# Kernel tuning notes

Measured on AMD Instinct MI355X. Metric: run time of the kernel, lower is better.

The kernel has to match this reference:

```python
import jax, jax.numpy as jnp
import numpy as np

N_EMBD = 1024
N_HEAD = 16
STRIDE = 128
C = 8
SEQ = 2048
BATCH = 2


def _sparse_causal_mask(nd, ns, stride, c, dtype):
    # Faithful vectorization of _sparse_attention_mask:
    # column j is globally visible if (j % stride) >= stride - c (the last c
    # columns of each stride block), each query also sees its own stride block,
    # and everything is causally masked (j <= q).
    j = jnp.arange(ns)
    q = jnp.arange(ns)[:, None]
    col_sel = (j % stride) >= (stride - c)          # strided summary columns
    same_block = (j[None, :] // stride) == (q // stride)  # local block
    causal = j[None, :] <= q
    mask = ((col_sel[None, :] | same_block) & causal).astype(dtype)
    return mask[ns - nd:]


def setup_inputs() -> dict:
    key = jax.random.key(0)
    k1, k2, k3 = jax.random.split(key, 3)
    inputs = jax.random.normal(k1, (BATCH, SEQ, N_EMBD), dtype=jnp.float32)
    w_attn = jax.random.normal(k2, (N_EMBD, 3 * N_EMBD), dtype=jnp.float32) * 0.02
    b_attn = jnp.zeros((3 * N_EMBD,), dtype=jnp.float32)
    proj_std = 0.02 / np.sqrt(2 * 24)  # n_layer = 24
    w_proj = jax.random.normal(k3, (N_EMBD, N_EMBD), dtype=jnp.float32) * proj_std
    b_proj = jnp.zeros((N_EMBD,), dtype=jnp.float32)
    return {"inputs": inputs, "w_attn": w_attn, "b_attn": b_attn,
            "w_proj": w_proj, "b_proj": b_proj}


def reference(inputs, w_attn, b_attn, w_proj, b_proj):
    B, S, E = inputs.shape
    H = N_HEAD
    D = E // H
    qkv = inputs @ w_attn + b_attn                     # [B,S,3E]
    q, k, v = jnp.split(qkv, 3, axis=-1)
    def split_heads(x):
        return x.reshape(B, S, H, D).transpose(0, 2, 1, 3)  # [B,H,S,D]
    q, k, v = split_heads(q), split_heads(k), split_heads(v)
    present = jnp.stack([k, v], axis=1)                # [B,2,H,S,D]
    scale = jnp.asarray(D, q.dtype) ** 0.5
    w = jnp.einsum('bhqd,bhkd->bhqk', q, k) / scale    # [B,H,S,S]
    mask = _sparse_causal_mask(S, S, STRIDE, C, w.dtype)
    w = w * mask - 1e10 * (1.0 - mask)
    p = jax.nn.softmax(w, axis=-1).astype(v.dtype)
    h = jnp.einsum('bhqk,bhkd->bhqd', p, v)            # [B,H,S,D]
    h = h.transpose(0, 2, 1, 3).reshape(B, S, E)       # merge heads
    h = h @ w_proj + b_proj
    # dropout p=0.0 (eval) -> identity
    return (h, present)
```

## Files before the change

kernel.cpp:

```cpp
#include <hip/hip_runtime.h>
#include <stdint.h>

typedef unsigned short u16;
typedef unsigned int u32;
typedef __attribute__((ext_vector_type(4))) float f32x4;
typedef __attribute__((ext_vector_type(4))) u16 u16x4;
typedef __attribute__((ext_vector_type(8))) __bf16 bf16x8;

__device__ __forceinline__ u16 f2bf(float f) {
  u32 u = __builtin_bit_cast(u32, f);
  u = (u + 0x7FFFu + ((u >> 16) & 1u)) >> 16;
  return (u16)u;
}

__device__ __forceinline__ void gload_lds16(const void* g, void* l) {
  __builtin_amdgcn_global_load_lds(
      (const __attribute__((address_space(1))) void*)(uintptr_t)(g),
      (__attribute__((address_space(3))) void*)(u32)(uintptr_t)(l),
      16, 0, 0);
}

__global__ __launch_bounds__(256) void k_prep(
    const float* __restrict__ x, u16* __restrict__ xbf,
    const float* __restrict__ wa, u16* __restrict__ wat,
    const float* __restrict__ wp, u16* __restrict__ wpt) {
  __shared__ float tile[32][33];
  const int bid = blockIdx.x, t = threadIdx.x;
  if (bid < 4096) {
    int i = bid * 256 + t;
    f32x4 v = ((const f32x4*)x)[i];
    u16x4 o = { f2bf(v.x), f2bf(v.y), f2bf(v.z), f2bf(v.w) };
    ((u16x4*)xbf)[i] = o;
    return;
  }
  const float* in;
  u16* out;
  int n0, k0, N;
  if (bid < 4096 + 3072) {
    int idx = bid - 4096;
    in = wa; out = wat; N = 3072;
    n0 = (idx % 96) * 32; k0 = (idx / 96) * 32;
  } else {
    int idx = bid - 7168;
    in = wp; out = wpt; N = 1024;
    n0 = (idx & 31) * 32; k0 = (idx >> 5) * 32;
  }
  int c = t & 31, r0 = t >> 5;
#pragma unroll
  for (int i = 0; i < 4; ++i)
    tile[r0 + i * 8][c] = in[(size_t)(k0 + r0 + i * 8) * N + n0 + c];
  __syncthreads();
  int on = t >> 3, ok = (t & 7) * 4;
  u16x4 o = { f2bf(tile[ok + 0][on]), f2bf(tile[ok + 1][on]),
              f2bf(tile[ok + 2][on]), f2bf(tile[ok + 3][on]) };
  *(u16x4*)&out[(size_t)(n0 + on) * 1024 + k0 + ok] = o;
}

__global__ __launch_bounds__(256) void k_kv(const float* __restrict__ present,
                                            u16* __restrict__ kbf,
                                            u16* __restrict__ vtw) {
  __shared__ float tile[32][33];
  const int bid = blockIdx.x, t = threadIdx.x;
  if (bid >= 4096) {
    int i = bid - 4096;
    size_t idx = (size_t)i * 256 + t;
    size_t b = idx >> 19, off = idx & ((1u << 19) - 1);
    f32x4 v = ((const f32x4*)present)[b * (1u << 20) + off];
    u16x4 o = { f2bf(v.x), f2bf(v.y), f2bf(v.z), f2bf(v.w) };
    ((u16x4*)kbf)[idx] = o;
    return;
  }
  int bh = bid >> 7, rem = bid & 127;
  int s0 = (rem >> 1) * 32, d0 = (rem & 1) * 32;
  int b = bh >> 4, h = bh & 15;
  const float* vsrc = present + (((size_t)(b * 2 + 1) * 16 + h) * 2048) * 64;
  u16* vdst = vtw + ((size_t)bh * 64) * 2048;
  int c = t & 31, r0 = t >> 5;
#pragma unroll
  for (int i = 0; i < 4; ++i)
    tile[r0 + i * 8][c] = vsrc[(size_t)(s0 + r0 + i * 8) * 64 + d0 + c];
  __syncthreads();
  int on = t >> 3, ok = (t & 7) * 4;
  u16x4 o = { f2bf(tile[ok + 0][on]), f2bf(tile[ok + 1][on]),
              f2bf(tile[ok + 2][on]), f2bf(tile[ok + 3][on]) };
  *(u16x4*)&vdst[(size_t)(d0 + on) * 2048 + s0 + ok] = o;
}

__global__ __launch_bounds__(512, 1) void k_gemm256(
    const u16* __restrict__ A, const u16* __restrict__ Bt,
    const float* __restrict__ bias, u16* __restrict__ outq,
    float* __restrict__ outp) {
  __shared__ u16 a_lds[2][256 * 64];
  __shared__ u16 b_lds[2][256 * 64];
  const int t = threadIdx.x;
  const int lane = t & 63, w = t >> 6;
  const int cc = lane & 15, g = lane >> 4;
  const int wr = w >> 2, wc = w & 3;

  int flat = blockIdx.y * 12 + blockIdx.x;
  flat = (flat & 7) * 24 + (flat >> 3);
  const int m0 = (flat / 12) * 256, n0 = (flat % 12) * 256;

  const int srow = t >> 3;
  const int scolb = (t & 7) * 16;
  const size_t pitch = 2048;

  auto stage = [&](int bi, int kt) {
#pragma unroll
    for (int hh = 0; hh < 2; ++hh)
#pragma unroll
      for (int i = 0; i < 2; ++i) {
        int row = hh * 128 + i * 64 + srow;
        int sw = scolb ^ ((row & 7) << 4);
        gload_lds16((const char*)A + (size_t)(m0 + row) * pitch + kt * 128 + sw,
                    (char*)a_lds[bi] + row * 128 + scolb);
        gload_lds16((const char*)Bt + (size_t)(n0 + row) * pitch + kt * 128 + sw,
                    (char*)b_lds[bi] + row * 128 + scolb);
      }
  };

  f32x4 acc[8][4] = {};

  stage(0, 0);
  stage(1, 1);
  __syncthreads();

  for (int kt = 0; kt < 16; ++kt) {
    const int bi = kt & 1;
    if (kt >= 1 && kt < 15) stage(1 - bi, kt + 1);

    bf16x8 bfr[4][2];
#pragma unroll
    for (int nf = 0; nf < 4; ++nf) {
      int row = wc * 64 + nf * 16 + cc;
#pragma unroll
      for (int kk = 0; kk < 2; ++kk)
        bfr[nf][kk] = *(const bf16x8*)((const char*)b_lds[bi] + row * 128 +
                                       ((kk * 64 + g * 16) ^ ((row & 7) << 4)));
    }
#pragma unroll
    for (int q = 0; q < 4; ++q) {
      bf16x8 af[2][2];
#pragma unroll
      for (int mf = 0; mf < 2; ++mf) {
        int row = wr * 128 + q * 32 + mf * 16 + cc;
#pragma unroll
        for (int kk = 0; kk < 2; ++kk)
          af[mf][kk] = *(const bf16x8*)((const char*)a_lds[bi] + row * 128 +
                                        ((kk * 64 + g * 16) ^ ((row & 7) << 4)));
      }
      __builtin_amdgcn_s_setprio(1);
#pragma unroll
      for (int mf = 0; mf < 2; ++mf)
#pragma unroll
        for (int nf = 0; nf < 4; ++nf)
#pragma unroll
          for (int kk = 0; kk < 2; ++kk)
            acc[q * 2 + mf][nf] = __builtin_amdgcn_mfma_f32_16x16x32_bf16(
                af[mf][kk], bfr[nf][kk], acc[q * 2 + mf][nf], 0, 0, 0);
      __builtin_amdgcn_s_setprio(0);
    }
    if (kt < 15) __syncthreads();
  }

  float bv[4];
#pragma unroll
  for (int nf = 0; nf < 4; ++nf) bv[nf] = bias[n0 + wc * 64 + nf * 16 + cc];

#pragma unroll
  for (int q8 = 0; q8 < 8; ++q8)
#pragma unroll
    for (int nf = 0; nf < 4; ++nf) {
      int n = n0 + wc * 64 + nf * 16 + cc;
      int mb = m0 + wr * 128 + q8 * 16 + g * 4;
      float v[4];
#pragma unroll
      for (int j = 0; j < 4; ++j) v[j] = acc[q8][nf][j] + bv[nf];
      if (n < 1024) {
#pragma unroll
        for (int j = 0; j < 4; ++j) outq[(size_t)(mb + j) * 1024 + n] = f2bf(v[j]);
      } else {
        int n2 = n - 1024;
        int kv = n2 >> 10; n2 &= 1023;
        int hh = n2 >> 6, d = n2 & 63;
        int bb = mb >> 11, ss = mb & 2047;
        float* pr = outp + ((((size_t)bb * 2 + kv) * 16 + hh) * 2048 + ss) * 64 + d;
#pragma unroll
        for (int j = 0; j < 4; ++j) pr[(size_t)j * 64] = v[j];
      }
    }
}

template <int EPI, int BN>
__global__ __launch_bounds__(256) void k_gemm(
    const u16* __restrict__ A, const u16* __restrict__ Bt,
    const float* __restrict__ bias, u16* __restrict__ outq,
    float* __restrict__ outp, int M, int N, int K) {
  __shared__ u16 a_lds[128 * 64];
  __shared__ u16 b_lds[BN * 64];
  const int t = threadIdx.x;
  const int lane = t & 63, w = t >> 6;
  const int m0 = blockIdx.y * 128, n0 = blockIdx.x * BN;
  const int srow = t >> 3;
  const int scb = (t & 7) * 16;
  const int ssw = scb ^ ((srow & 7) << 4);
  const size_t pitch = (size_t)K * 2;
  const char* aS = (const char*)A + (size_t)(m0 + srow) * pitch + ssw;
  const char* bS = (const char*)Bt + (size_t)(n0 + srow) * pitch + ssw;
  char* al = (char*)a_lds + t * 16;
  char* bl = (char*)b_lds + t * 16;
  const int wm = (w >> 1) * 64, wn = (w & 1) * (BN / 2);
  const int cc = lane & 15, g = lane >> 4;
  constexpr int NF = BN / 32;

  f32x4 acc[4][NF] = {};

  for (int kt = 0; kt < K; kt += 64) {
    __syncthreads();
#pragma unroll
    for (int i = 0; i < 4; ++i)
      gload_lds16(aS + (size_t)kt * 2 + (size_t)i * 32 * pitch, al + i * 4096);
#pragma unroll
    for (int i = 0; i < BN / 32; ++i)
      gload_lds16(bS + (size_t)kt * 2 + (size_t)i * 32 * pitch, bl + i * 4096);
    __syncthreads();
#pragma unroll
    for (int kk = 0; kk < 2; ++kk) {
      bf16x8 af[4], bf_[NF];
#pragma unroll
      for (int mf = 0; mf < 4; ++mf) {
        int row = wm + mf * 16 + cc;
        af[mf] = *(const bf16x8*)((const char*)a_lds + row * 128 +
                                  ((kk * 64 + g * 16) ^ ((row & 7) << 4)));
      }
#pragma unroll
      for (int nf = 0; nf < NF; ++nf) {
        int row = wn + nf * 16 + cc;
        bf_[nf] = *(const bf16x8*)((const char*)b_lds + row * 128 +
                                   ((kk * 64 + g * 16) ^ ((row & 7) << 4)));
      }
#pragma unroll
      for (int mf = 0; mf < 4; ++mf)
#pragma unroll
        for (int nf = 0; nf < NF; ++nf)
          acc[mf][nf] = __builtin_amdgcn_mfma_f32_16x16x32_bf16(
              af[mf], bf_[nf], acc[mf][nf], 0, 0, 0);
    }
  }

  float bv[NF];
#pragma unroll
  for (int nf = 0; nf < NF; ++nf) bv[nf] = bias[n0 + wn + nf * 16 + cc];

#pragma unroll
  for (int mf = 0; mf < 4; ++mf)
#pragma unroll
    for (int nf = 0; nf < NF; ++nf) {
      int n = n0 + wn + nf * 16 + cc;
      int mb = m0 + wm + mf * 16 + g * 4;
      float v[4];
#pragma unroll
      for (int j = 0; j < 4; ++j) v[j] = acc[mf][nf][j] + bv[nf];
      if (EPI == 1) {
#pragma unroll
        for (int j = 0; j < 4; ++j) outp[(size_t)(mb + j) * N + n] = v[j];
      } else if (n < 1024) {
#pragma unroll
        for (int j = 0; j < 4; ++j) outq[(size_t)(mb + j) * 1024 + n] = f2bf(v[j]);
      } else {
        int n2 = n - 1024;
        int kv = n2 >> 10; n2 &= 1023;
        int hh = n2 >> 6, d = n2 & 63;
        int bb = mb >> 11, ss = mb & 2047;
        float* pr = outp + ((((size_t)bb * 2 + kv) * 16 + hh) * 2048 + ss) * 64 + d;
#pragma unroll
        for (int j = 0; j < 4; ++j) pr[(size_t)j * 64] = v[j];
      }
    }
}

__global__ __launch_bounds__(256) void k_attn(
    const u16* __restrict__ qws, const u16* __restrict__ kbf,
    const u16* __restrict__ vtw, u16* __restrict__ hws) {
  const int qb = blockIdx.x, h = blockIdx.y, b = blockIdx.z;
  const int t = threadIdx.x, lane = t & 63, w = t >> 6;
  const int cc = lane & 15, g = lane >> 4;

  __shared__ u16 k_lds[256 * 64];
  __shared__ u16 p_lds[4][32 * 72];
  __shared__ float rsum[4][32];

  const char* kh = (const char*)kbf + (size_t)(b * 16 + h) * (2048 * 128);
  const char* vh = (const char*)vtw + (size_t)(b * 16 + h) * (64 * 4096);

  {
    int rr = t >> 3, seg = (t & 7) * 16;
#pragma unroll
    for (int i = 0; i < 8; ++i) {
      int r = i * 32 + rr;
      int i2 = r - 128;
      int gr = (r < 128) ? (qb * 128 + r) : ((i2 >> 3) * 128 + 120 + (i2 & 7));
      gload_lds16(kh + (size_t)gr * 128 + (seg ^ ((r & 7) << 4)),
                  (char*)k_lds + i * 4096 + t * 16);
    }
  }

  bf16x8 qf_[2][2];
  {
    const char* qsrc = (const char*)qws +
        (size_t)(b * 2048 + qb * 128 + w * 32 + cc) * 2048 + h * 128 + g * 16;
#pragma unroll
    for (int qf = 0; qf < 2; ++qf)
#pragma unroll
      for (int kk = 0; kk < 2; ++kk)
        qf_[qf][kk] = *(const bf16x8*)(qsrc + (size_t)qf * 16 * 2048 + kk * 64);
  }
  __syncthreads();

  const int nsum = 8 * qb;
  f32x4 o_[2][4] = {};
  float lsum[2] = { 0.f, 0.f };

#pragma unroll 2
  for (int ch = 0; ch < 4; ++ch) {
    f32x4 s[4][2] = {};
#pragma unroll
    for (int kf2 = 0; kf2 < 4; ++kf2) {
      int row = ch * 64 + kf2 * 16 + cc;
      const char* kr = (const char*)k_lds + row * 128;
#pragma unroll
      for (int kk = 0; kk < 2; ++kk) {
        bf16x8 kfr = *(const bf16x8*)(kr + ((kk * 64 + g * 16) ^ ((cc & 7) << 4)));
#pragma unroll
        for (int qf = 0; qf < 2; ++qf)
          s[kf2][qf] = __builtin_amdgcn_mfma_f32_16x16x32_bf16(
              kfr, qf_[qf][kk], s[kf2][qf], 0, 0, 0);
      }
    }
#pragma unroll
    for (int qf = 0; qf < 2; ++qf) {
      int q_local = w * 32 + qf * 16 + cc;
#pragma unroll
      for (int kf2 = 0; kf2 < 4; ++kf2) {
#pragma unroll
        for (int j = 0; j < 4; ++j) {
          int key = ch * 64 + kf2 * 16 + g * 4 + j;
          bool vis = (key < 128) ? (key <= q_local) : (key - 128 < nsum);
          float p = vis ? exp2f(s[kf2][qf][j] * 0.180336884f) : 0.f;
          s[kf2][qf][j] = p;
          lsum[qf] += p;
        }
        u16x4 pw = { f2bf(s[kf2][qf][0]), f2bf(s[kf2][qf][1]),
                     f2bf(s[kf2][qf][2]), f2bf(s[kf2][qf][3]) };
        *(u16x4*)&p_lds[w][(qf * 16 + cc) * 72 + kf2 * 16 + g * 4] = pw;
      }
    }
#pragma unroll
    for (int kk = 0; kk < 2; ++kk) {
      bf16x8 pa[2], vb[4];
#pragma unroll
      for (int mf = 0; mf < 2; ++mf)
        pa[mf] = *(const bf16x8*)((const char*)p_lds[w] +
                                  (mf * 16 + cc) * 144 + kk * 64 + g * 16);
      int cb = (ch < 2) ? (qb * 256 + ch * 128 + kk * 64 + g * 16)
                        : (((ch - 2) * 8 + kk * 4 + g) * 256 + 240);
#pragma unroll
      for (int nf = 0; nf < 4; ++nf)
        vb[nf] = *(const bf16x8*)(vh + (size_t)(nf * 16 + cc) * 4096 + cb);
#pragma unroll
      for (int mf = 0; mf < 2; ++mf)
#pragma unroll
        for (int nf = 0; nf < 4; ++nf)
          o_[mf][nf] = __builtin_amdgcn_mfma_f32_16x16x32_bf16(pa[mf], vb[nf],
                                                               o_[mf][nf], 0, 0, 0);
    }
  }

#pragma unroll
  for (int qf = 0; qf < 2; ++qf) {
    float sum = lsum[qf];
    sum += __shfl_xor(sum, 16);
    sum += __shfl_xor(sum, 32);
    if (g == 0) rsum[w][qf * 16 + cc] = sum;
  }
#pragma unroll
  for (int mf = 0; mf < 2; ++mf)
#pragma unroll
    for (int j = 0; j < 4; ++j) {
      float inv = 1.0f / rsum[w][mf * 16 + g * 4 + j];
      size_t row = (size_t)(b * 2048 + qb * 128 + w * 32 + mf * 16 + g * 4 + j);
#pragma unroll
      for (int nf = 0; nf < 4; ++nf)
        hws[row * 1024 + h * 64 + nf * 16 + cc] = f2bf(o_[mf][nf][j] * inv);
    }
}

extern "C" void kernel_launch(void* const* d_in, const int* in_sizes, int n_in,
                              void* d_out, int out_size, void* d_ws, size_t ws_size,
                              hipStream_t stream) {
  const float* x      = (const float*)d_in[0];
  const float* w_attn = (const float*)d_in[1];
  const float* b_attn = (const float*)d_in[2];
  const float* w_proj = (const float*)d_in[3];
  const float* b_proj = (const float*)d_in[4];
  float* h_out   = (float*)d_out;
  float* present = (float*)d_out + 4194304;

  char* ws = (char*)d_ws;
  u16* xbf = (u16*)(ws);
  u16* qws = (u16*)(ws + (8u << 20));
  u16* wat = (u16*)(ws + (16u << 20));
  u16* wpt = (u16*)(ws + (22u << 20));
  u16* kbf = (u16*)(ws + (24u << 20));
  u16* vtw = (u16*)(ws + (32u << 20));
  u16* hws = xbf;

  k_prep<<<8192, 256, 0, stream>>>(x, xbf, w_attn, wat, w_proj, wpt);
  k_gemm256<<<dim3(12, 16), 512, 0, stream>>>(xbf, wat, b_attn, qws, present);
  k_kv<<<8192, 256, 0, stream>>>(present, kbf, vtw);
  k_attn<<<dim3(16, 16, 2), 256, 0, stream>>>(qws, kbf, vtw, hws);
  k_gemm<1, 64><<<dim3(16, 32), 256, 0, stream>>>(hws, wpt, b_proj, nullptr,
                                                  h_out, 4096, 1024, 1024);
}
```

Before: 92.40 us.

## Retile QKV GEMM to 256x192 with split A/B staging and XCD-aware mapping

The QKV projection GEMM moves from 256x256 tiles (192 blocks) to 256x192 tiles (256 blocks), so the grid matches the 256 CUs more evenly. Staging is split so B loads for the next k-step are issued before compute and A loads are issued midway through the MFMA loop. Explicit vmcnt waits plus s_barrier replace __syncthreads, giving finer overlap of loads with math. Block-to-tile mapping is remapped to be XCD-aware (chiplet-aware) for both GEMMs, to improve L2 locality. The risk is a fragile hand-written waitcnt schedule, and the output-projection GEMM remap depends on the grid shape.

```diff
diff --git a/kernel.cpp b/kernel.cpp
--- a/kernel.cpp
+++ b/kernel.cpp
@@ -91,55 +91,65 @@
     const float* __restrict__ bias, u16* __restrict__ outq,
     float* __restrict__ outp) {
   __shared__ u16 a_lds[2][256 * 64];
-  __shared__ u16 b_lds[2][256 * 64];
+  __shared__ u16 b_lds[2][192 * 64];
   const int t = threadIdx.x;
   const int lane = t & 63, w = t >> 6;
   const int cc = lane & 15, g = lane >> 4;
   const int wr = w >> 2, wc = w & 3;
 
-  int flat = blockIdx.y * 12 + blockIdx.x;
-  flat = (flat & 7) * 24 + (flat >> 3);
-  const int m0 = (flat / 12) * 256, n0 = (flat % 12) * 256;
+  int f = blockIdx.y * 16 + blockIdx.x;
+  int xcd = f & 7, idx = f >> 3;
+  const int m0 = ((xcd >> 1) * 4 + (idx >> 3)) * 256;
+  const int n0 = ((xcd & 1) * 8 + (idx & 7)) * 192;
 
   const int srow = t >> 3;
   const int scolb = (t & 7) * 16;
   const size_t pitch = 2048;
 
-  auto stage = [&](int bi, int kt) {
-#pragma unroll
-    for (int hh = 0; hh < 2; ++hh)
-#pragma unroll
-      for (int i = 0; i < 2; ++i) {
-        int row = hh * 128 + i * 64 + srow;
-        int sw = scolb ^ ((row & 7) << 4);
-        gload_lds16((const char*)A + (size_t)(m0 + row) * pitch + kt * 128 + sw,
-                    (char*)a_lds[bi] + row * 128 + scolb);
-        gload_lds16((const char*)Bt + (size_t)(n0 + row) * pitch + kt * 128 + sw,
-                    (char*)b_lds[bi] + row * 128 + scolb);
-      }
+  auto stageB = [&](int bi, int kt) {
+#pragma unroll
+    for (int i = 0; i < 3; ++i) {
+      int row = i * 64 + srow;
+      gload_lds16((const char*)Bt + (size_t)(n0 + row) * pitch + kt * 128 +
+                      (scolb ^ ((row & 7) << 4)),
+                  (char*)b_lds[bi] + row * 128 + scolb);
+    }
   };
-
-  f32x4 acc[8][4] = {};
-
-  stage(0, 0);
-  stage(1, 1);
-  __syncthreads();
-
-  for (int kt = 0; kt < 16; ++kt) {
-    const int bi = kt & 1;
-    if (kt >= 1 && kt < 15) stage(1 - bi, kt + 1);
-
-    bf16x8 bfr[4][2];
-#pragma unroll
-    for (int nf = 0; nf < 4; ++nf) {
-      int row = wc * 64 + nf * 16 + cc;
+  auto stageA = [&](int bi, int kt) {
+#pragma unroll
+    for (int i = 0; i < 4; ++i) {
+      int row = i * 64 + srow;
+      gload_lds16((const char*)A + (size_t)(m0 + row) * pitch + kt * 128 +
+                      (scolb ^ ((row & 7) << 4)),
+                  (char*)a_lds[bi] + row * 128 + scolb);
+    }
+  };
+
+  f32x4 acc[8][3] = {};
+
+  stageB(0, 0);
+  stageA(0, 0);
+
+  for (int j = 0; j < 16; ++j) {
+    const int bi = j & 1, nx = bi ^ 1;
+    if (j < 15) {
+      stageB(nx, j + 1);
+      asm volatile("s_waitcnt vmcnt(3)\n\ts_barrier" ::: "memory");
+    } else {
+      asm volatile("s_waitcnt vmcnt(0)\n\ts_barrier" ::: "memory");
+    }
+
+    bf16x8 bfr[3][2];
+#pragma unroll
+    for (int nf = 0; nf < 3; ++nf) {
+      int row = wc * 48 + nf * 16 + cc;
 #pragma unroll
       for (int kk = 0; kk < 2; ++kk)
         bfr[nf][kk] = *(const bf16x8*)((const char*)b_lds[bi] + row * 128 +
                                        ((kk * 64 + g * 16) ^ ((row & 7) << 4)));
     }
 #pragma unroll
-    for (int q = 0; q < 4; ++q) {
+    for (int q = 0; q < 2; ++q) {
       bf16x8 af[2][2];
 #pragma unroll
       for (int mf = 0; mf < 2; ++mf) {
@@ -153,29 +163,56 @@
 #pragma unroll
       for (int mf = 0; mf < 2; ++mf)
 #pragma unroll
-        for (int nf = 0; nf < 4; ++nf)
+        for (int nf = 0; nf < 3; ++nf)
 #pragma unroll
           for (int kk = 0; kk < 2; ++kk)
             acc[q * 2 + mf][nf] = __builtin_amdgcn_mfma_f32_16x16x32_bf16(
                 af[mf][kk], bfr[nf][kk], acc[q * 2 + mf][nf], 0, 0, 0);
       __builtin_amdgcn_s_setprio(0);
     }
-    if (kt < 15) __syncthreads();
-  }
-
-  float bv[4];
-#pragma unroll
-  for (int nf = 0; nf < 4; ++nf) bv[nf] = bias[n0 + wc * 64 + nf * 16 + cc];
-
-#pragma unroll
-  for (int q8 = 0; q8 < 8; ++q8)
-#pragma unroll
-    for (int nf = 0; nf < 4; ++nf) {
-      int n = n0 + wc * 64 + nf * 16 + cc;
-      int mb = m0 + wr * 128 + q8 * 16 + g * 4;
+
+    if (j < 15) stageA(nx, j + 1);
+
+#pragma unroll
+    for (int q = 2; q < 4; ++q) {
+      bf16x8 af[2][2];
+#pragma unroll
+      for (int mf = 0; mf < 2; ++mf) {
+        int row = wr * 128 + q * 32 + mf * 16 + cc;
+#pragma unroll
+        for (int kk = 0; kk < 2; ++kk)
+          af[mf][kk] = *(const bf16x8*)((const char*)a_lds[bi] + row * 128 +
+                                        ((kk * 64 + g * 16) ^ ((row & 7) << 4)));
+      }
+      __builtin_amdgcn_s_setprio(1);
+#pragma unroll
+      for (int mf = 0; mf < 2; ++mf)
+#pragma unroll
+        for (int nf = 0; nf < 3; ++nf)
+#pragma unroll
+          for (int kk = 0; kk < 2; ++kk)
+            acc[q * 2 + mf][nf] = __builtin_amdgcn_mfma_f32_16x16x32_bf16(
+                af[mf][kk], bfr[nf][kk], acc[q * 2 + mf][nf], 0, 0, 0);
+      __builtin_amdgcn_s_setprio(0);
+    }
+
+    if (j < 15)
+      asm volatile("s_waitcnt vmcnt(4)\n\ts_barrier" ::: "memory");
+  }
+
+  float bv[3];
+#pragma unroll
+  for (int nf = 0; nf < 3; ++nf) bv[nf] = bias[n0 + wc * 48 + nf * 16 + cc];
+
+#pragma unroll
+  for (int mf = 0; mf < 8; ++mf)
+#pragma unroll
+    for (int nf = 0; nf < 3; ++nf) {
+      int n = n0 + wc * 48 + nf * 16 + cc;
+      int mb = m0 + wr * 128 + mf * 16 + g * 4;
       float v[4];
 #pragma unroll
-      for (int j = 0; j < 4; ++j) v[j] = acc[q8][nf][j] + bv[nf];
+      for (int j = 0; j < 4; ++j) v[j] = acc[mf][nf][j] + bv[nf];
       if (n < 1024) {
 #pragma unroll
         for (int j = 0; j < 4; ++j) outq[(size_t)(mb + j) * 1024 + n] = f2bf(v[j]);
@@ -200,7 +237,19 @@
   __shared__ u16 b_lds[BN * 64];
   const int t = threadIdx.x;
   const int lane = t & 63, w = t >> 6;
-  const int m0 = blockIdx.y * 128, n0 = blockIdx.x * BN;
+
+  int m0, n0;
+  {
+    constexpr int NXT = (EPI == 0) ? 24 : 16;
+    constexpr int NCH = (EPI == 0) ? 12 : 8;
+    int f = blockIdx.y * NXT + blockIdx.x;
+    int xcd = f & 7, idx = f >> 3;
+    int mt = (xcd >> 1) * 8 + idx / NCH;
+    int nt = (xcd & 1) * NCH + idx % NCH;
+    m0 = mt * 128;
+    n0 = nt * BN;
+  }
+
   const int srow = t >> 3;
   const int scb = (t & 7) * 16;
   const int ssw = scb ^ ((srow & 7) << 4);
@@ -416,7 +465,7 @@
   u16* hws = xbf;
 
   k_prep<<<8192, 256, 0, stream>>>(x, xbf, w_attn, wat, w_proj, wpt);
-  k_gemm256<<<dim3(12, 16), 512, 0, stream>>>(xbf, wat, b_attn, qws, present);
+  k_gemm256<<<dim3(16, 16), 512, 0, stream>>>(xbf, wat, b_attn, qws, present);
   k_kv<<<8192, 256, 0, stream>>>(present, kbf, vtw);
   k_attn<<<dim3(16, 16, 2), 256, 0, stream>>>(qws, kbf, vtw, hws);
   k_gemm<1, 64><<<dim3(16, 32), 256, 0, stream>>>(hws, wpt, b_proj, nullptr,
```

After: 87.05 us. 1.06x faster.
